# Performance work log

Hardware: AMD Instinct MI355X
Metric: run time of the kernel (lower is better)

The kernel has to match this reference:

```python
import jax, jax.numpy as jnp
import numpy as np

N_NODES = 50000
N_EDGES = 800000
D = 128
N_RELS = 460  # 2 * num_rels
N_BASES = 32
SUBMAT = D // N_BASES  # 4
INV_TEMP = 0.1


def setup_inputs() -> dict:
    key = jax.random.key(0)
    ks = jax.random.split(key, 16)
    return {
        "h": jax.random.normal(ks[0], (N_NODES, D), jnp.float32),
        "first_prev": jax.random.normal(ks[1], (N_NODES, D), jnp.float32),
        "second_prev": jax.random.normal(ks[2], (N_NODES, D), jnp.float32),
        "time_diff": jax.random.uniform(ks[3], (N_NODES, 1), jnp.float32),
        "edge_src": jax.random.randint(ks[4], (N_EDGES,), 0, N_NODES, jnp.int32),
        "edge_dst": jax.random.randint(ks[5], (N_EDGES,), 0, N_NODES, jnp.int32),
        "edge_type": jax.random.randint(ks[6], (N_EDGES,), 0, N_RELS, jnp.int32),
        "edge_norm": jax.random.uniform(ks[7], (N_EDGES, 1), jnp.float32),
        "node_norm": jax.random.uniform(ks[8], (N_NODES, 1), jnp.float32),
        "W1": jax.random.normal(ks[9], (N_RELS, N_BASES * SUBMAT * SUBMAT), jnp.float32) * 0.05,
        "W2": jax.random.normal(ks[10], (N_RELS, N_BASES * SUBMAT * SUBMAT), jnp.float32) * 0.05,
        "loop_w1": jax.random.normal(ks[11], (D, D), jnp.float32) * 0.05,
        "loop_w2": jax.random.normal(ks[12], (D, D), jnp.float32) * 0.05,
        "time_w1": jax.random.normal(ks[13], (D, D), jnp.float32) * 0.05,
        "time_w2": jax.random.normal(ks[14], (D, D), jnp.float32) * 0.05,
    }


def _drgcn_layer(h, prev, time_diff, W, loop_w, time_w,
                 edge_src, edge_dst, edge_type, edge_norm, node_norm, activate):
    n = h.shape[0]
    # self-loop message (dropout is identity in eval)
    loop_msg = h @ loop_w                                     # [N, D]
    # block-diagonal per-edge message: gather relation blocks + batched small matmul
    w = W[edge_type].reshape(-1, N_BASES, SUBMAT, SUBMAT)     # [E, B, si, so]
    hs = h[edge_src].reshape(-1, N_BASES, SUBMAT)             # [E, B, si]
    msg = jnp.einsum('ebi,ebio->ebo', hs, w).reshape(-1, h.shape[1])  # [E, D]
    msg = msg * edge_norm                                     # per-edge norm
    agg = jax.ops.segment_sum(msg, edge_dst, num_segments=n)  # scatter-sum to dst
    agg = agg * node_norm                                     # apply_func node norm
    # time-decay residual + self-loop (bias=None in this config)
    out = agg + (prev @ time_w) * jnp.exp(-time_diff * INV_TEMP) + loop_msg
    if activate:
        out = jax.nn.relu(out)
    return out


def reference(h, first_prev, second_prev, time_diff,
              edge_src, edge_dst, edge_type, edge_norm, node_norm,
              W1, W2, loop_w1, loop_w2, time_w1, time_w2):
    h1 = _drgcn_layer(h, first_prev, time_diff, W1, loop_w1, time_w1,
                      edge_src, edge_dst, edge_type, edge_norm, node_norm, activate=False)
    h2 = _drgcn_layer(h1, second_prev, time_diff, W2, loop_w2, time_w2,
                      edge_src, edge_dst, edge_type, edge_norm, node_norm, activate=True)
    return (h1, h2)
```

## Files before the change

kernel.cpp:

```cpp
#include <hip/hip_runtime.h>

#define NN 50000
#define NE 800000
#define DD 128
#define NPAD 50176
#define NBLK_SCAN 196

typedef __attribute__((ext_vector_type(8))) short short8;
typedef __attribute__((ext_vector_type(4))) float f32x4;

static __device__ __forceinline__ float b2f(unsigned short u) {
    return __builtin_bit_cast(float, (unsigned)u << 16);
}
static __device__ __forceinline__ unsigned short f2b(float f) {
    unsigned u = __builtin_bit_cast(unsigned, f);
    u += 0x7FFFu + ((u >> 16) & 1u);
    return (unsigned short)(u >> 16);
}

__global__ __launch_bounds__(256) void k_hist(
    const int* __restrict__ edst, int* __restrict__ cnt)
{
    const int e = blockIdx.x * 256 + threadIdx.x;
    atomicAdd(&cnt[edst[e]], 1);
}

__global__ __launch_bounds__(256) void k_scan_a(
    const int* __restrict__ cnt, int* __restrict__ bsum)
{
    __shared__ int s[256];
    const int t = threadIdx.x;
    s[t] = cnt[blockIdx.x * 256 + t];
    __syncthreads();
    for (int d = 128; d > 0; d >>= 1) {
        if (t < d) s[t] += s[t + d];
        __syncthreads();
    }
    if (t == 0) bsum[blockIdx.x] = s[0];
}

__global__ __launch_bounds__(256) void k_scan_b(int* __restrict__ bsum)
{
    __shared__ int s[256];
    const int t = threadIdx.x;
    s[t] = (t < NBLK_SCAN) ? bsum[t] : 0;
    __syncthreads();
    for (int d = 1; d < 256; d <<= 1) {
        int v = (t >= d) ? s[t - d] : 0;
        __syncthreads();
        s[t] += v;
        __syncthreads();
    }
    bsum[t] = (t == 0) ? 0 : s[t - 1];
}

__global__ __launch_bounds__(256) void k_scan_c(
    const int* __restrict__ cnt, const int* __restrict__ bsum,
    int* __restrict__ off, int* __restrict__ cur)
{
    __shared__ int s[256];
    const int t = threadIdx.x;
    const int i = blockIdx.x * 256 + t;
    const int c = cnt[i];
    s[t] = c;
    __syncthreads();
    for (int d = 1; d < 256; d <<= 1) {
        int v = (t >= d) ? s[t - d] : 0;
        __syncthreads();
        s[t] += v;
        __syncthreads();
    }
    const int ex = bsum[blockIdx.x] + s[t] - c;
    off[i] = ex;
    cur[i] = ex;
}

__global__ __launch_bounds__(256) void k_scatter(
    const int* __restrict__ esrc, const int* __restrict__ edst,
    const int* __restrict__ etyp, const float* __restrict__ enorm,
    int* __restrict__ cur, int2* __restrict__ ssrc_type,
    float* __restrict__ snorm)
{
    const int e = blockIdx.x * 256 + threadIdx.x;
    const int pos = atomicAdd(&cur[edst[e]], 1);
    ssrc_type[pos] = make_int2(esrc[e], etyp[e]);
    snorm[pos] = enorm[e];
}

__global__ __launch_bounds__(256) void conv_x_full(
    const float* __restrict__ x, const float* __restrict__ prev,
    const float* __restrict__ tdiff, unsigned short* __restrict__ X)
{
    const int idx = blockIdx.x * 256 + threadIdx.x;
    const int n = idx >> 7, j = idx & 127;
    const float d = __expf(-tdiff[n] * 0.1f);
    X[(size_t)n * 256 + j]       = f2b(x[(size_t)n * 128 + j]);
    X[(size_t)n * 256 + 128 + j] = f2b(prev[(size_t)n * 128 + j] * d);
}

__global__ __launch_bounds__(256) void conv_x_right(
    const float* __restrict__ prev, const float* __restrict__ tdiff,
    unsigned short* __restrict__ X)
{
    const int idx = blockIdx.x * 256 + threadIdx.x;
    const int n = idx >> 7, j = idx & 127;
    const float d = __expf(-tdiff[n] * 0.1f);
    X[(size_t)n * 256 + 128 + j] = f2b(prev[(size_t)n * 128 + j] * d);
}

__global__ __launch_bounds__(256) void conv_w(
    const float* __restrict__ W, unsigned short* __restrict__ Wb)
{
    const int i = blockIdx.x * 256 + threadIdx.x;
    Wb[i] = f2b(W[i]);
}

__global__ __launch_bounds__(256) void pack_wc(
    const float* __restrict__ lw, const float* __restrict__ tw,
    unsigned short* __restrict__ Wp)
{
    const int c = blockIdx.x * 256 + threadIdx.x;
    const int ct = c >> 9, ks = (c >> 6) & 7, lane = c & 63;
    const int col = ct * 16 + (lane & 15);
    unsigned short* o = Wp + (size_t)c * 8;
    #pragma unroll
    for (int i = 0; i < 8; ++i) {
        const int k = ks * 32 + (lane >> 4) * 8 + i;
        const float v = (k < 128) ? lw[(size_t)k * 128 + col]
                                  : tw[(size_t)(k - 128) * 128 + col];
        o[i] = f2b(v);
    }
}

__device__ __forceinline__ float pick4(float4 v, int o) {
    float a = (o & 1) ? v.y : v.x;
    float b = (o & 1) ? v.w : v.z;
    return (o & 2) ? b : a;
}

__global__ __launch_bounds__(256) void k_agg_b(
    const unsigned short* __restrict__ x,
    const int2*  __restrict__ ssrc_type,
    const float* __restrict__ snorm,
    const int*   __restrict__ off,
    const unsigned short* __restrict__ Wb,
    float*       __restrict__ agg)
{
    const int lane = threadIdx.x & 63;
    const int n    = blockIdx.x * 4 + (threadIdx.x >> 6);

    const int beg = off[n];
    const int end = off[n + 1];

    float4 acca = make_float4(0.f, 0.f, 0.f, 0.f);
    float4 accb = make_float4(0.f, 0.f, 0.f, 0.f);

    for (int i = beg; i < end; ++i) {
        const int2  st = ssrc_type[i];
        const float nr = snorm[i];
        const unsigned short* wr = Wb + (size_t)st.y * 512 + 4 * lane;
        const ushort4 wa = *(const ushort4*)wr;
        const ushort4 wb = *(const ushort4*)(wr + 256);
        const unsigned short* hr = x + (size_t)st.x * 256;
        const float ha = b2f(hr[lane]) * nr;
        const float hb = b2f(hr[64 + lane]) * nr;
        acca.x += ha * b2f(wa.x); acca.y += ha * b2f(wa.y);
        acca.z += ha * b2f(wa.z); acca.w += ha * b2f(wa.w);
        accb.x += hb * b2f(wb.x); accb.y += hb * b2f(wb.y);
        accb.z += hb * b2f(wb.z); accb.w += hb * b2f(wb.w);
    }

    #pragma unroll
    for (int d = 1; d <= 2; d <<= 1) {
        acca.x += __shfl_xor(acca.x, d); acca.y += __shfl_xor(acca.y, d);
        acca.z += __shfl_xor(acca.z, d); acca.w += __shfl_xor(acca.w, d);
        accb.x += __shfl_xor(accb.x, d); accb.y += __shfl_xor(accb.y, d);
        accb.z += __shfl_xor(accb.z, d); accb.w += __shfl_xor(accb.w, d);
    }

    const int o = lane & 3;
    agg[(size_t)n * DD + lane]      = pick4(acca, o);
    agg[(size_t)n * DD + 64 + lane] = pick4(accb, o);
}

template<int ACT, int WRITE_NEXT>
__global__ __launch_bounds__(256) void combine_mfma(
    const float* __restrict__ agg,
    const unsigned short* __restrict__ X,
    const unsigned short* __restrict__ Wp,
    const float* __restrict__ nnorm,
    float* __restrict__ out,
    unsigned short* __restrict__ Xnext)
{
    const int t = threadIdx.x;
    const int l = t & 63;
    const int w = t >> 6;
    const int wr = w >> 1, wc = w & 1;
    const int l15 = l & 15, lhi = l >> 4;
    const int rowbase = blockIdx.x * 64 + wr * 32;

    f32x4 acc[2][4] = {};

    const int ar0 = min(rowbase + l15, NN - 1);
    const int ar1 = min(rowbase + 16 + l15, NN - 1);
    const unsigned short* a0p = X + (size_t)ar0 * 256 + lhi * 8;
    const unsigned short* a1p = X + (size_t)ar1 * 256 + lhi * 8;
    const unsigned short* bp  = Wp + (size_t)(wc * 4) * 8 * 512 + (size_t)l * 8;

    #pragma unroll
    for (int ks = 0; ks < 8; ++ks) {
        const short8 a0 = *(const short8*)(a0p + ks * 32);
        const short8 a1 = *(const short8*)(a1p + ks * 32);
        #pragma unroll
        for (int ct = 0; ct < 4; ++ct) {
            const short8 b = *(const short8*)(bp + (size_t)(ct * 8 + ks) * 512);
            acc[0][ct] = __builtin_amdgcn_mfma_f32_16x16x32_bf16(a0, b, acc[0][ct], 0, 0, 0);
            acc[1][ct] = __builtin_amdgcn_mfma_f32_16x16x32_bf16(a1, b, acc[1][ct], 0, 0, 0);
        }
    }

    #pragma unroll
    for (int rg = 0; rg < 2; ++rg) {
        #pragma unroll
        for (int q = 0; q < 4; ++q) {
            const int row = rowbase + rg * 16 + lhi * 4 + q;
            if (row < NN) {
                const float nn = nnorm[row];
                #pragma unroll
                for (int ct = 0; ct < 4; ++ct) {
                    const int col = wc * 64 + ct * 16 + l15;
                    float v = agg[(size_t)row * DD + col] * nn + acc[rg][ct][q];
                    if (ACT) v = fmaxf(v, 0.f);
                    out[(size_t)row * DD + col] = v;
                    if (WRITE_NEXT) Xnext[(size_t)row * 256 + col] = f2b(v);
                }
            }
        }
    }
}

__global__ __launch_bounds__(256) void k_agg(
    const float* __restrict__ x, const int2* __restrict__ ssrc_type,
    const float* __restrict__ snorm, const int* __restrict__ off,
    const float* __restrict__ W, float* __restrict__ agg)
{
    const int lane = threadIdx.x & 63;
    const int n    = blockIdx.x * 4 + (threadIdx.x >> 6);
    const int beg = off[n], end = off[n + 1];
    float4 acca = make_float4(0.f, 0.f, 0.f, 0.f);
    float4 accb = make_float4(0.f, 0.f, 0.f, 0.f);
    for (int i = beg; i < end; ++i) {
        const int2  st = ssrc_type[i];
        const float nr = snorm[i];
        const float* wr = W + (size_t)st.y * 512 + 4 * lane;
        const float4 wa = *(const float4*)wr;
        const float4 wb = *(const float4*)(wr + 256);
        const float* hr = x + (size_t)st.x * DD;
        const float ha = hr[lane] * nr;
        const float hb = hr[64 + lane] * nr;
        acca.x += ha * wa.x; acca.y += ha * wa.y; acca.z += ha * wa.z; acca.w += ha * wa.w;
        accb.x += hb * wb.x; accb.y += hb * wb.y; accb.z += hb * wb.z; accb.w += hb * wb.w;
    }
    #pragma unroll
    for (int d = 1; d <= 2; d <<= 1) {
        acca.x += __shfl_xor(acca.x, d); acca.y += __shfl_xor(acca.y, d);
        acca.z += __shfl_xor(acca.z, d); acca.w += __shfl_xor(acca.w, d);
        accb.x += __shfl_xor(accb.x, d); accb.y += __shfl_xor(accb.y, d);
        accb.z += __shfl_xor(accb.z, d); accb.w += __shfl_xor(accb.w, d);
    }
    const int o = lane & 3;
    agg[(size_t)n * DD + lane]      = pick4(acca, o);
    agg[(size_t)n * DD + 64 + lane] = pick4(accb, o);
}

__global__ __launch_bounds__(256) void edge_msg(
    const float* __restrict__ x, const int* __restrict__ esrc,
    const int* __restrict__ edst, const int* __restrict__ etyp,
    const float* __restrict__ enorm, const float* __restrict__ W,
    float* __restrict__ agg)
{
    const int t  = threadIdx.x;
    const int le = t >> 7;
    const int j  = t & 127;
    const int e  = blockIdx.x * 2 + le;
    __shared__ float sh[2][DD];
    sh[le][j] = x[(size_t)esrc[e] * DD + j];
    __syncthreads();
    const int b = j >> 2, o = j & 3;
    const float* wr = W + (size_t)etyp[e] * 512 + b * 16 + o;
    const float4 hv = *(const float4*)&sh[le][b * 4];
    float m = hv.x * wr[0] + hv.y * wr[4] + hv.z * wr[8] + hv.w * wr[12];
    m *= enorm[e];
    atomicAdd(&agg[(size_t)edst[e] * DD + j], m);
}

template<int ACT>
__global__ __launch_bounds__(256) void combine(
    float* __restrict__ out, const float* __restrict__ x,
    const float* __restrict__ prev, const float* __restrict__ tdiff,
    const float* __restrict__ nnorm, const float* __restrict__ lw,
    const float* __restrict__ tw)
{
    const int t = threadIdx.x;
    const int j = t & 127;
    const int r = t >> 7;
    const int base = blockIdx.x * 8;
    __shared__ float sh[8][DD];
    __shared__ float sp[8][DD];
    #pragma unroll
    for (int q = 0; q < 4; ++q) {
        const int m = q * 2 + r;
        const int n = base + m;
        const float decay = __expf(-tdiff[n] * 0.1f);
        sh[m][j] = x[(size_t)n * DD + j];
        sp[m][j] = prev[(size_t)n * DD + j] * decay;
    }
    __syncthreads();
    float acc[4] = {0.f, 0.f, 0.f, 0.f};
    for (int k = 0; k < DD; k += 4) {
        float wl[4], wt[4];
        #pragma unroll
        for (int kk = 0; kk < 4; ++kk) {
            wl[kk] = lw[(size_t)(k + kk) * DD + j];
            wt[kk] = tw[(size_t)(k + kk) * DD + j];
        }
        #pragma unroll
        for (int q = 0; q < 4; ++q) {
            const int m = q * 2 + r;
            const float4 a = *(const float4*)&sh[m][k];
            const float4 p = *(const float4*)&sp[m][k];
            acc[q] += a.x * wl[0] + a.y * wl[1] + a.z * wl[2] + a.w * wl[3]
                    + p.x * wt[0] + p.y * wt[1] + p.z * wt[2] + p.w * wt[3];
        }
    }
    #pragma unroll
    for (int q = 0; q < 4; ++q) {
        const int m = q * 2 + r;
        const int n = base + m;
        float v = out[(size_t)n * DD + j] * nnorm[n] + acc[q];
        if (ACT) v = fmaxf(v, 0.f);
        out[(size_t)n * DD + j] = v;
    }
}

extern "C" void kernel_launch(void* const* d_in, const int* in_sizes, int n_in,
                              void* d_out, int out_size, void* d_ws, size_t ws_size,
                              hipStream_t stream) {
    const float* h     = (const float*)d_in[0];
    const float* fprev = (const float*)d_in[1];
    const float* sprev = (const float*)d_in[2];
    const float* tdiff = (const float*)d_in[3];
    const int*   esrc  = (const int*)d_in[4];
    const int*   edst  = (const int*)d_in[5];
    const int*   etyp  = (const int*)d_in[6];
    const float* enorm = (const float*)d_in[7];
    const float* nnorm = (const float*)d_in[8];
    const float* W1    = (const float*)d_in[9];
    const float* W2    = (const float*)d_in[10];
    const float* lw1   = (const float*)d_in[11];
    const float* lw2   = (const float*)d_in[12];
    const float* tw1   = (const float*)d_in[13];
    const float* tw2   = (const float*)d_in[14];

    float* h1 = (float*)d_out;
    float* h2 = h1 + (size_t)NN * DD;
    const size_t layer_bytes = (size_t)NN * DD * sizeof(float);

    char* wsp = (char*)d_ws;
    int*   cnt       = (int*)wsp;   wsp += (size_t)NPAD * 4;
    int*   off       = (int*)wsp;   wsp += (size_t)NPAD * 4;
    int*   cur       = (int*)wsp;   wsp += (size_t)NPAD * 4;
    int*   bsum      = (int*)wsp;   wsp += 256 * 4;
    int2*  ssrc_type = (int2*)wsp;  wsp += (size_t)NE * 8;
    float* snorm     = (float*)wsp; wsp += (size_t)NE * 4;
    const size_t ws_sorted = (size_t)(wsp - (char*)d_ws);
    unsigned short* X1   = (unsigned short*)wsp; wsp += (size_t)NN * 256 * 2;
    unsigned short* X2   = (unsigned short*)wsp; wsp += (size_t)NN * 256 * 2;
    unsigned short* Wc1p = (unsigned short*)wsp; wsp += 4096 * 8 * 2;
    unsigned short* Wc2p = (unsigned short*)wsp; wsp += 4096 * 8 * 2;
    unsigned short* W1b  = (unsigned short*)wsp; wsp += (size_t)460 * 512 * 2;
    unsigned short* W2b  = (unsigned short*)wsp; wsp += (size_t)460 * 512 * 2;
    const size_t ws_full = (size_t)(wsp - (char*)d_ws);

    const int grid_mm = (NN + 63) / 64;

    if (ws_size >= ws_full) {
        hipMemsetAsync(cnt, 0, (size_t)NPAD * 4, stream);
        k_hist   <<<NE / 256, 256, 0, stream>>>(edst, cnt);
        k_scan_a <<<NBLK_SCAN, 256, 0, stream>>>(cnt, bsum);
        k_scan_b <<<1, 256, 0, stream>>>(bsum);
        k_scan_c <<<NBLK_SCAN, 256, 0, stream>>>(cnt, bsum, off, cur);
        k_scatter<<<NE / 256, 256, 0, stream>>>(esrc, edst, etyp, enorm,
                                                cur, ssrc_type, snorm);
        conv_x_full <<<NN * DD / 256, 256, 0, stream>>>(h, fprev, tdiff, X1);
        conv_x_right<<<NN * DD / 256, 256, 0, stream>>>(sprev, tdiff, X2);
        pack_wc<<<16, 256, 0, stream>>>(lw1, tw1, Wc1p);
        pack_wc<<<16, 256, 0, stream>>>(lw2, tw2, Wc2p);
        conv_w <<<460 * 512 / 256, 256, 0, stream>>>(W1, W1b);
        conv_w <<<460 * 512 / 256, 256, 0, stream>>>(W2, W2b);
        k_agg_b<<<NN / 4, 256, 0, stream>>>(X1, ssrc_type, snorm, off, W1b, h1);
        combine_mfma<0, 1><<<grid_mm, 256, 0, stream>>>(h1, X1, Wc1p, nnorm, h1, X2);
        k_agg_b<<<NN / 4, 256, 0, stream>>>(X2, ssrc_type, snorm, off, W2b, h2);
        combine_mfma<1, 0><<<grid_mm, 256, 0, stream>>>(h2, X2, Wc2p, nnorm, h2, nullptr);
    } else if (ws_size >= ws_sorted) {
        hipMemsetAsync(cnt, 0, (size_t)NPAD * 4, stream);
        k_hist   <<<NE / 256, 256, 0, stream>>>(edst, cnt);
        k_scan_a <<<NBLK_SCAN, 256, 0, stream>>>(cnt, bsum);
        k_scan_b <<<1, 256, 0, stream>>>(bsum);
        k_scan_c <<<NBLK_SCAN, 256, 0, stream>>>(cnt, bsum, off, cur);
        k_scatter<<<NE / 256, 256, 0, stream>>>(esrc, edst, etyp, enorm,
                                                cur, ssrc_type, snorm);
        k_agg<<<NN / 4, 256, 0, stream>>>(h, ssrc_type, snorm, off, W1, h1);
        combine<0><<<NN / 8, 256, 0, stream>>>(h1, h, fprev, tdiff, nnorm, lw1, tw1);
        k_agg<<<NN / 4, 256, 0, stream>>>(h1, ssrc_type, snorm, off, W2, h2);
        combine<1><<<NN / 8, 256, 0, stream>>>(h2, h1, sprev, tdiff, nnorm, lw2, tw2);
    } else {
        hipMemsetAsync(h1, 0, layer_bytes, stream);
        edge_msg<<<NE / 2, 256, 0, stream>>>(h, esrc, edst, etyp, enorm, W1, h1);
        combine<0><<<NN / 8, 256, 0, stream>>>(h1, h, fprev, tdiff, nnorm, lw1, tw1);
        hipMemsetAsync(h2, 0, layer_bytes, stream);
        edge_msg<<<NE / 2, 256, 0, stream>>>(h1, esrc, edst, etyp, enorm, W2, h2);
        combine<1><<<NN / 8, 256, 0, stream>>>(h2, h1, sprev, tdiff, nnorm, lw2, tw2);
    }
}
```

Baseline: 522.6 us.

## Pack sorted edges into int4, rework aggregation lane mapping, fuse prep kernels

Sorted edge records (src, type, norm) are packed into one 16-byte int4 so each edge costs one load. The aggregation kernel gives each lane two adjacent bf16 inputs, loaded as one 32-bit read, and a 16-byte weight vector. It unrolls four edges into independent accumulators, cuts the cross-lane reduction to a single shuffle, and moves the node-norm multiply into aggregation. The conversion and packing kernels for both layers are merged to cut launch count. Edge storage grows from 12 to 16 bytes per edge, and the scalar readfirstlane assumes every lane in a wave reads the same edge.

```diff
diff --git a/kernel.cpp b/kernel.cpp
--- a/kernel.cpp
+++ b/kernel.cpp
@@ -11,6 +11,12 @@
 
 static __device__ __forceinline__ float b2f(unsigned short u) {
     return __builtin_bit_cast(float, (unsigned)u << 16);
+}
+static __device__ __forceinline__ float b2f_lo(unsigned u) {
+    return __builtin_bit_cast(float, u << 16);
+}
+static __device__ __forceinline__ float b2f_hi(unsigned u) {
+    return __builtin_bit_cast(float, u & 0xffff0000u);
 }
 static __device__ __forceinline__ unsigned short f2b(float f) {
     unsigned u = __builtin_bit_cast(unsigned, f);
@@ -78,48 +84,46 @@
 __global__ __launch_bounds__(256) void k_scatter(
     const int* __restrict__ esrc, const int* __restrict__ edst,
     const int* __restrict__ etyp, const float* __restrict__ enorm,
-    int* __restrict__ cur, int2* __restrict__ ssrc_type,
-    float* __restrict__ snorm)
+    int* __restrict__ cur, int4* __restrict__ sedge)
 {
     const int e = blockIdx.x * 256 + threadIdx.x;
     const int pos = atomicAdd(&cur[edst[e]], 1);
-    ssrc_type[pos] = make_int2(esrc[e], etyp[e]);
-    snorm[pos] = enorm[e];
-}
-
-__global__ __launch_bounds__(256) void conv_x_full(
-    const float* __restrict__ x, const float* __restrict__ prev,
-    const float* __restrict__ tdiff, unsigned short* __restrict__ X)
+    sedge[pos] = make_int4(esrc[e], etyp[e],
+                           __builtin_bit_cast(int, enorm[e]), 0);
+}
+
+__global__ __launch_bounds__(256) void conv_x(
+    const float* __restrict__ x, const float* __restrict__ fprev,
+    const float* __restrict__ sprev, const float* __restrict__ tdiff,
+    unsigned short* __restrict__ X1, unsigned short* __restrict__ X2)
 {
     const int idx = blockIdx.x * 256 + threadIdx.x;
     const int n = idx >> 7, j = idx & 127;
     const float d = __expf(-tdiff[n] * 0.1f);
-    X[(size_t)n * 256 + j]       = f2b(x[(size_t)n * 128 + j]);
-    X[(size_t)n * 256 + 128 + j] = f2b(prev[(size_t)n * 128 + j] * d);
-}
-
-__global__ __launch_bounds__(256) void conv_x_right(
-    const float* __restrict__ prev, const float* __restrict__ tdiff,
-    unsigned short* __restrict__ X)
-{
-    const int idx = blockIdx.x * 256 + threadIdx.x;
-    const int n = idx >> 7, j = idx & 127;
-    const float d = __expf(-tdiff[n] * 0.1f);
-    X[(size_t)n * 256 + 128 + j] = f2b(prev[(size_t)n * 128 + j] * d);
-}
-
-__global__ __launch_bounds__(256) void conv_w(
-    const float* __restrict__ W, unsigned short* __restrict__ Wb)
+    X1[(size_t)n * 256 + j]       = f2b(x[(size_t)n * 128 + j]);
+    X1[(size_t)n * 256 + 128 + j] = f2b(fprev[(size_t)n * 128 + j] * d);
+    X2[(size_t)n * 256 + 128 + j] = f2b(sprev[(size_t)n * 128 + j] * d);
+}
+
+__global__ __launch_bounds__(256) void conv_w2(
+    const float* __restrict__ W1, const float* __restrict__ W2,
+    unsigned short* __restrict__ W1b, unsigned short* __restrict__ W2b)
 {
     const int i = blockIdx.x * 256 + threadIdx.x;
-    Wb[i] = f2b(W[i]);
-}
-
-__global__ __launch_bounds__(256) void pack_wc(
-    const float* __restrict__ lw, const float* __restrict__ tw,
-    unsigned short* __restrict__ Wp)
-{
-    const int c = blockIdx.x * 256 + threadIdx.x;
+    if (i < 460 * 512) W1b[i] = f2b(W1[i]);
+    else               W2b[i - 460 * 512] = f2b(W2[i - 460 * 512]);
+}
+
+__global__ __launch_bounds__(256) void pack_wc2(
+    const float* __restrict__ lw1, const float* __restrict__ tw1,
+    const float* __restrict__ lw2, const float* __restrict__ tw2,
+    unsigned short* __restrict__ Wp1, unsigned short* __restrict__ Wp2)
+{
+    const int g = blockIdx.x * 256 + threadIdx.x;
+    const int c = g & 4095;
+    const float* lw = (g < 4096) ? lw1 : lw2;
+    const float* tw = (g < 4096) ? tw1 : tw2;
+    unsigned short* Wp = (g < 4096) ? Wp1 : Wp2;
     const int ct = c >> 9, ks = (c >> 6) & 7, lane = c & 63;
     const int col = ct * 16 + (lane & 15);
     unsigned short* o = Wp + (size_t)c * 8;
@@ -132,55 +136,65 @@
     }
 }
 
-__device__ __forceinline__ float pick4(float4 v, int o) {
-    float a = (o & 1) ? v.y : v.x;
-    float b = (o & 1) ? v.w : v.z;
-    return (o & 2) ? b : a;
-}
-
-__global__ __launch_bounds__(256) void k_agg_b(
+__device__ __forceinline__ void agg_edge(
     const unsigned short* __restrict__ x,
-    const int2*  __restrict__ ssrc_type,
-    const float* __restrict__ snorm,
+    const unsigned short* __restrict__ Wb,
+    const int4* __restrict__ sedge, int i,
+    int woff, int l, float4& acc)
+{
+    const int4 e = sedge[i];
+    const int src = __builtin_amdgcn_readfirstlane(e.x);
+    const int typ = __builtin_amdgcn_readfirstlane(e.y);
+    const float nr = __builtin_bit_cast(float, __builtin_amdgcn_readfirstlane(e.z));
+    const unsigned hw = ((const unsigned*)(x + (size_t)src * 256))[l];
+    const uint4 wv = *(const uint4*)(Wb + (size_t)typ * 512 + woff);
+    const float h0 = b2f_lo(hw) * nr;
+    const float h1 = b2f_hi(hw) * nr;
+    acc.x += h0 * b2f_lo(wv.x) + h1 * b2f_lo(wv.z);
+    acc.y += h0 * b2f_hi(wv.x) + h1 * b2f_hi(wv.z);
+    acc.z += h0 * b2f_lo(wv.y) + h1 * b2f_lo(wv.w);
+    acc.w += h0 * b2f_hi(wv.y) + h1 * b2f_hi(wv.w);
+}
+
+__global__ __launch_bounds__(256) void k_agg2(
+    const unsigned short* __restrict__ x,
+    const int4*  __restrict__ sedge,
     const int*   __restrict__ off,
     const unsigned short* __restrict__ Wb,
+    const float* __restrict__ nnorm,
     float*       __restrict__ agg)
 {
-    const int lane = threadIdx.x & 63;
-    const int n    = blockIdx.x * 4 + (threadIdx.x >> 6);
-
-    const int beg = off[n];
-    const int end = off[n + 1];
-
-    float4 acca = make_float4(0.f, 0.f, 0.f, 0.f);
-    float4 accb = make_float4(0.f, 0.f, 0.f, 0.f);
-
-    for (int i = beg; i < end; ++i) {
-        const int2  st = ssrc_type[i];
-        const float nr = snorm[i];
-        const unsigned short* wr = Wb + (size_t)st.y * 512 + 4 * lane;
-        const ushort4 wa = *(const ushort4*)wr;
-        const ushort4 wb = *(const ushort4*)(wr + 256);
-        const unsigned short* hr = x + (size_t)st.x * 256;
-        const float ha = b2f(hr[lane]) * nr;
-        const float hb = b2f(hr[64 + lane]) * nr;
-        acca.x += ha * b2f(wa.x); acca.y += ha * b2f(wa.y);
-        acca.z += ha * b2f(wa.z); acca.w += ha * b2f(wa.w);
-        accb.x += hb * b2f(wb.x); accb.y += hb * b2f(wb.y);
-        accb.z += hb * b2f(wb.z); accb.w += hb * b2f(wb.w);
-    }
-
-    #pragma unroll
-    for (int d = 1; d <= 2; d <<= 1) {
-        acca.x += __shfl_xor(acca.x, d); acca.y += __shfl_xor(acca.y, d);
-        acca.z += __shfl_xor(acca.z, d); acca.w += __shfl_xor(acca.w, d);
-        accb.x += __shfl_xor(accb.x, d); accb.y += __shfl_xor(accb.y, d);
-        accb.z += __shfl_xor(accb.z, d); accb.w += __shfl_xor(accb.w, d);
-    }
-
-    const int o = lane & 3;
-    agg[(size_t)n * DD + lane]      = pick4(acca, o);
-    agg[(size_t)n * DD + 64 + lane] = pick4(accb, o);
+    const int l = threadIdx.x & 63;
+    const int n = blockIdx.x * 4 + (threadIdx.x >> 6);
+    const int beg = off[n], end = off[n + 1];
+    const int woff = (l >> 1) * 16 + (l & 1) * 8;
+
+    float4 a0 = {0,0,0,0}, a1 = {0,0,0,0}, a2 = {0,0,0,0}, a3 = {0,0,0,0};
+
+    int i = beg;
+    for (; i + 4 <= end; i += 4) {
+        agg_edge(x, Wb, sedge, i,     woff, l, a0);
+        agg_edge(x, Wb, sedge, i + 1, woff, l, a1);
+        agg_edge(x, Wb, sedge, i + 2, woff, l, a2);
+        agg_edge(x, Wb, sedge, i + 3, woff, l, a3);
+    }
+    for (; i < end; ++i) agg_edge(x, Wb, sedge, i, woff, l, a0);
+
+    float4 s;
+    s.x = (a0.x + a1.x) + (a2.x + a3.x);
+    s.y = (a0.y + a1.y) + (a2.y + a3.y);
+    s.z = (a0.z + a1.z) + (a2.z + a3.z);
+    s.w = (a0.w + a1.w) + (a2.w + a3.w);
+    s.x += __shfl_xor(s.x, 1);
+    s.y += __shfl_xor(s.y, 1);
+    s.z += __shfl_xor(s.z, 1);
+    s.w += __shfl_xor(s.w, 1);
+
+    const float nn = nnorm[n];
+    const float e0 = (l & 1) ? s.z : s.x;
+    const float e1 = (l & 1) ? s.w : s.y;
+    float2* outp = (float2*)(agg + (size_t)n * DD + (l >> 1) * 4 + (l & 1) * 2);
+    *outp = make_float2(e0 * nn, e1 * nn);
 }
 
 template<int ACT, int WRITE_NEXT>
@@ -188,7 +202,6 @@
     const float* __restrict__ agg,
     const unsigned short* __restrict__ X,
     const unsigned short* __restrict__ Wp,
-    const float* __restrict__ nnorm,
     float* __restrict__ out,
     unsigned short* __restrict__ Xnext)
 {
@@ -225,11 +238,10 @@
         for (int q = 0; q < 4; ++q) {
             const int row = rowbase + rg * 16 + lhi * 4 + q;
             if (row < NN) {
-                const float nn = nnorm[row];
                 #pragma unroll
                 for (int ct = 0; ct < 4; ++ct) {
                     const int col = wc * 64 + ct * 16 + l15;
-                    float v = agg[(size_t)row * DD + col] * nn + acc[rg][ct][q];
+                    float v = agg[(size_t)row * DD + col] + acc[rg][ct][q];
                     if (ACT) v = fmaxf(v, 0.f);
                     out[(size_t)row * DD + col] = v;
                     if (WRITE_NEXT) Xnext[(size_t)row * 256 + col] = f2b(v);
@@ -239,10 +251,16 @@
     }
 }
 
-__global__ __launch_bounds__(256) void k_agg(
-    const float* __restrict__ x, const int2* __restrict__ ssrc_type,
-    const float* __restrict__ snorm, const int* __restrict__ off,
-    const float* __restrict__ W, float* __restrict__ agg)
+__device__ __forceinline__ float pick4(float4 v, int o) {
+    float a = (o & 1) ? v.y : v.x;
+    float b = (o & 1) ? v.w : v.z;
+    return (o & 2) ? b : a;
+}
+
+__global__ __launch_bounds__(256) void k_agg_t2(
+    const float* __restrict__ x, const int4* __restrict__ sedge,
+    const int* __restrict__ off, const float* __restrict__ W,
+    float* __restrict__ agg)
 {
     const int lane = threadIdx.x & 63;
     const int n    = blockIdx.x * 4 + (threadIdx.x >> 6);
@@ -250,12 +268,12 @@
     float4 acca = make_float4(0.f, 0.f, 0.f, 0.f);
     float4 accb = make_float4(0.f, 0.f, 0.f, 0.f);
     for (int i = beg; i < end; ++i) {
-        const int2  st = ssrc_type[i];
-        const float nr = snorm[i];
-        const float* wr = W + (size_t)st.y * 512 + 4 * lane;
+        const int4 e = sedge[i];
+        const float nr = __builtin_bit_cast(float, e.z);
+        const float* wr = W + (size_t)e.y * 512 + 4 * lane;
         const float4 wa = *(const float4*)wr;
         const float4 wb = *(const float4*)(wr + 256);
-        const float* hr = x + (size_t)st.x * DD;
+        const float* hr = x + (size_t)e.x * DD;
         const float ha = hr[lane] * nr;
         const float hb = hr[64 + lane] * nr;
         acca.x += ha * wa.x; acca.y += ha * wa.y; acca.z += ha * wa.z; acca.w += ha * wa.w;
@@ -367,12 +385,11 @@
     const size_t layer_bytes = (size_t)NN * DD * sizeof(float);
 
     char* wsp = (char*)d_ws;
-    int*   cnt       = (int*)wsp;   wsp += (size_t)NPAD * 4;
-    int*   off       = (int*)wsp;   wsp += (size_t)NPAD * 4;
-    int*   cur       = (int*)wsp;   wsp += (size_t)NPAD * 4;
-    int*   bsum      = (int*)wsp;   wsp += 256 * 4;
-    int2*  ssrc_type = (int2*)wsp;  wsp += (size_t)NE * 8;
-    float* snorm     = (float*)wsp; wsp += (size_t)NE * 4;
+    int*   cnt   = (int*)wsp;  wsp += (size_t)NPAD * 4;
+    int*   off   = (int*)wsp;  wsp += (size_t)NPAD * 4;
+    int*   cur   = (int*)wsp;  wsp += (size_t)NPAD * 4;
+    int*   bsum  = (int*)wsp;  wsp += 256 * 4;
+    int4*  sedge = (int4*)wsp; wsp += (size_t)NE * 16;
     const size_t ws_sorted = (size_t)(wsp - (char*)d_ws);
     unsigned short* X1   = (unsigned short*)wsp; wsp += (size_t)NN * 256 * 2;
     unsigned short* X2   = (unsigned short*)wsp; wsp += (size_t)NN * 256 * 2;
@@ -390,29 +407,24 @@
         k_scan_a <<<NBLK_SCAN, 256, 0, stream>>>(cnt, bsum);
         k_scan_b <<<1, 256, 0, stream>>>(bsum);
         k_scan_c <<<NBLK_SCAN, 256, 0, stream>>>(cnt, bsum, off, cur);
-        k_scatter<<<NE / 256, 256, 0, stream>>>(esrc, edst, etyp, enorm,
-                                                cur, ssrc_type, snorm);
-        conv_x_full <<<NN * DD / 256, 256, 0, stream>>>(h, fprev, tdiff, X1);
-        conv_x_right<<<NN * DD / 256, 256, 0, stream>>>(sprev, tdiff, X2);
-        pack_wc<<<16, 256, 0, stream>>>(lw1, tw1, Wc1p);
-        pack_wc<<<16, 256, 0, stream>>>(lw2, tw2, Wc2p);
-        conv_w <<<460 * 512 / 256, 256, 0, stream>>>(W1, W1b);
-        conv_w <<<460 * 512 / 256, 256, 0, stream>>>(W2, W2b);
-        k_agg_b<<<NN / 4, 256, 0, stream>>>(X1, ssrc_type, snorm, off, W1b, h1);
-        combine_mfma<0, 1><<<grid_mm, 256, 0, stream>>>(h1, X1, Wc1p, nnorm, h1, X2);
-        k_agg_b<<<NN / 4, 256, 0, stream>>>(X2, ssrc_type, snorm, off, W2b, h2);
-        combine_mfma<1, 0><<<grid_mm, 256, 0, stream>>>(h2, X2, Wc2p, nnorm, h2, nullptr);
+        k_scatter<<<NE / 256, 256, 0, stream>>>(esrc, edst, etyp, enorm, cur, sedge);
+        conv_x  <<<NN * DD / 256, 256, 0, stream>>>(h, fprev, sprev, tdiff, X1, X2);
+        conv_w2 <<<2 * 460 * 512 / 256, 256, 0, stream>>>(W1, W2, W1b, W2b);
+        pack_wc2<<<32, 256, 0, stream>>>(lw1, tw1, lw2, tw2, Wc1p, Wc2p);
+        k_agg2<<<NN / 4, 256, 0, stream>>>(X1, sedge, off, W1b, nnorm, h1);
+        combine_mfma<0, 1><<<grid_mm, 256, 0, stream>>>(h1, X1, Wc1p, h1, X2);
+        k_agg2<<<NN / 4, 256, 0, stream>>>(X2, sedge, off, W2b, nnorm, h2);
+        combine_mfma<1, 0><<<grid_mm, 256, 0, stream>>>(h2, X2, Wc2p, h2, nullptr);
     } else if (ws_size >= ws_sorted) {
         hipMemsetAsync(cnt, 0, (size_t)NPAD * 4, stream);
         k_hist   <<<NE / 256, 256, 0, stream>>>(edst, cnt);
         k_scan_a <<<NBLK_SCAN, 256, 0, stream>>>(cnt, bsum);
         k_scan_b <<<1, 256, 0, stream>>>(bsum);
         k_scan_c <<<NBLK_SCAN, 256, 0, stream>>>(cnt, bsum, off, cur);
-        k_scatter<<<NE / 256, 256, 0, stream>>>(esrc, edst, etyp, enorm,
-                                                cur, ssrc_type, snorm);
-        k_agg<<<NN / 4, 256, 0, stream>>>(h, ssrc_type, snorm, off, W1, h1);
+        k_scatter<<<NE / 256, 256, 0, stream>>>(esrc, edst, etyp, enorm, cur, sedge);
+        k_agg_t2<<<NN / 4, 256, 0, stream>>>(h, sedge, off, W1, h1);
         combine<0><<<NN / 8, 256, 0, stream>>>(h1, h, fprev, tdiff, nnorm, lw1, tw1);
-        k_agg<<<NN / 4, 256, 0, stream>>>(h1, ssrc_type, snorm, off, W2, h2);
+        k_agg_t2<<<NN / 4, 256, 0, stream>>>(h1, sedge, off, W2, h2);
         combine<1><<<NN / 8, 256, 0, stream>>>(h2, h1, sprev, tdiff, nnorm, lw2, tw2);
     } else {
         hipMemsetAsync(h1, 0, layer_bytes, stream);
```

Result: faster. 429.8 us (-17.8%).
